# Performance work log

Hardware: AMD Instinct MI355X
Metric: run time of the kernel (lower is better)

Reference implementation:

```python
import jax, jax.numpy as jnp
import numpy as np

B, S, D = 4, 2048, 1024  # batch, seq_len, d_model == d_internal


def setup_inputs() -> dict:
    key = jax.random.key(0)
    ks = jax.random.split(key, 7)
    s = 1.0 / np.sqrt(D)  # scale weights so softmax / relu stay in a sane range
    return {
        "input_vecs": jax.random.normal(ks[0], (B, S, D), jnp.float32),
        "Wq": jax.random.normal(ks[1], (D, D), jnp.float32) * s,
        "Wk": jax.random.normal(ks[2], (D, D), jnp.float32) * s,
        "Wv": jax.random.normal(ks[3], (D, D), jnp.float32) * s,
        "W1": jax.random.normal(ks[4], (D, D), jnp.float32) * s,  # linear1: d_internal -> d_model
        "b1": jnp.zeros((D,), jnp.float32),
        "W2": jax.random.normal(ks[5], (D, D), jnp.float32) * s,  # linear2: d_model -> d_internal
        "b2": jnp.zeros((D,), jnp.float32),
    }


def reference(input_vecs, Wq, Wk, Wv, W1, b1, W2, b2):
    d_internal = Wq.shape[1]
    # single-head self-attention: Q,K,V = X @ Wq/Wk/Wv
    q = jnp.einsum("bsd,de->bse", input_vecs, Wq)
    k = jnp.einsum("bsd,de->bse", input_vecs, Wk)
    v = jnp.einsum("bsd,de->bse", input_vecs, Wv)
    scores = jnp.einsum("bqe,bke->bqk", q, k) / jnp.sqrt(jnp.asarray(d_internal, q.dtype))
    attn = jax.nn.softmax(scores, axis=-1)               # [B, S, S]
    attn_out = jnp.einsum("bqk,bke->bqe", attn, v)       # [B, S, D]
    h = attn_out + input_vecs                            # residual 1
    h = jax.nn.relu(h @ W1 + b1)                         # linear1 + relu
    out = h @ W2 + b2 + input_vecs                       # linear2 + residual 2
    return out, attn
```

## Files before the change

kernel.cpp:

```cpp
#include <hip/hip_runtime.h>
#include <hip/hip_bf16.h>

typedef unsigned short u16;
typedef unsigned int   u32;
typedef u16   u16x8 __attribute__((ext_vector_type(8)));
typedef u16   u16x4 __attribute__((ext_vector_type(4)));
typedef __bf16 bf16x8 __attribute__((ext_vector_type(8)));
typedef float f32x4 __attribute__((ext_vector_type(4)));

__device__ __forceinline__ u16 f2bf(float f) {
    u32 u = __float_as_uint(f);
    u = u + 0x7FFFu + ((u >> 16) & 1u);
    return (u16)(u >> 16);
}
__device__ __forceinline__ float bf2f(u16 b) {
    return __uint_as_float((u32)b << 16);
}

__device__ __forceinline__ void gload16(const u16* g, u16* l) {
    __builtin_amdgcn_global_load_lds(
        (const __attribute__((address_space(1))) void*)g,
        (__attribute__((address_space(3))) void*)l,
        16, 0, 0);
}

#define WAITV(N) asm volatile("s_waitcnt vmcnt(" #N ")" ::: "memory")
#define SCHEDB() __builtin_amdgcn_sched_barrier(0)
#define BAR()    __builtin_amdgcn_s_barrier()

__global__ __launch_bounds__(256) void cvt_x(const float* __restrict__ X,
                                             u16* __restrict__ Xb) {
    const long i = (long)(blockIdx.x * 256 + threadIdx.x) * 8;
    float4 a = *(const float4*)(X + i);
    float4 b = *(const float4*)(X + i + 4);
    u16x8 r;
    r[0] = f2bf(a.x); r[1] = f2bf(a.y); r[2] = f2bf(a.z); r[3] = f2bf(a.w);
    r[4] = f2bf(b.x); r[5] = f2bf(b.y); r[6] = f2bf(b.z); r[7] = f2bf(b.w);
    *(u16x8*)(Xb + i) = r;
}

__global__ __launch_bounds__(256) void cvt_wT(const float* __restrict__ w0,
                                              const float* __restrict__ w1,
                                              const float* __restrict__ w2,
                                              const float* __restrict__ w3,
                                              const float* __restrict__ w4,
                                              u16* __restrict__ wt) {
    const float* srcs[5] = {w0, w1, w2, w3, w4};
    const float* W = srcs[blockIdx.z];
    u16* WT = wt + (long)blockIdx.z * 1048576;
    __shared__ float t[32][33];
    const int tx = threadIdx.x, ty = threadIdx.y;
    const int n0 = blockIdx.x * 32, k0 = blockIdx.y * 32;
    #pragma unroll
    for (int r = 0; r < 4; ++r)
        t[ty + 8 * r][tx] = W[(long)(k0 + ty + 8 * r) * 1024 + n0 + tx];
    __syncthreads();
    #pragma unroll
    for (int r = 0; r < 4; ++r)
        WT[(long)(n0 + ty + 8 * r) * 1024 + k0 + tx] = f2bf(t[tx][ty + 8 * r]);
}

enum { EPI_QKV = 0, EPI_ADDX_BF16 = 3,
       EPI_BIAS_RELU_BF16 = 4, EPI_BIAS_ADDX_F32 = 5 };

#define BM3 256
#define BN3 128
#define BK3 32
#define S3_A (BM3 * BK3)
#define S3_B (BN3 * BK3)
#define S3SZ (S3_A + S3_B)

__global__ __launch_bounds__(512, 2)
void gemm_bt32(const u16* __restrict__ A, const u16* __restrict__ Bt,
               void* __restrict__ Cout, void* __restrict__ CoutK,
               void* __restrict__ CoutV,
               const int M, const int N, const int K,
               const long sA, const long sB,
               const float scale) {
    const int GX = gridDim.x, GY = gridDim.y;
    const int p  = blockIdx.x + GX * (blockIdx.y + GY * blockIdx.z);
    const int slab = (p & 7) + 8 * (p / (8 * GY));
    const int vy   = (p >> 3) % GY;
    const int vx   = slab % GX;
    const int bz   = slab / GX;

    const u16* Ab = A + (long)bz * sA;
    const u16* Bb = Bt + (long)bz * sB;

    const int tid  = threadIdx.x;
    const int lane = tid & 63;
    const int w    = tid >> 6;
    const int wrg  = (w >> 1) * 64;
    const int wcg  = (w & 1) * 64;
    const int m0   = vx * BM3;
    const int n0   = vy * BN3;

    __shared__ __align__(16) u16 LDS[3 * S3SZ];

    f32x4 acc[4][4] = {};

    const long Kl = K;
    const int schunk = ((lane & 3) ^ ((lane >> 3) & 3)) * 8;
    const u16* Ag = Ab + (long)(m0 + w * 32 + (lane >> 2)) * Kl + schunk;
    const u16* Bg = Bb + (long)(n0 + w * 16 + (lane >> 2)) * Kl + schunk;

    const int rbase = lane & 15;
    const int koff  = ((lane >> 4) ^ ((rbase >> 1) & 3)) * 8;

    const int dAoff = (w * 32) * BK3;
    const int dBoff = S3_A + (w * 16) * BK3;

    #define LDA3(mi) (*(const bf16x8*)(Asl + (wrg + (mi) * 16 + rbase) * BK3 + koff))
    #define LDB3(ni) (*(const bf16x8*)(Bsl + (wcg + (ni) * 16 + rbase) * BK3 + koff))
    #define STAGE3(KT, SLOT) do {                                  \
        u16* a_ = &LDS[(SLOT) * S3SZ + dAoff];                     \
        u16* b_ = &LDS[(SLOT) * S3SZ + dBoff];                     \
        gload16(Ag + (KT), a_);                                    \
        gload16(Ag + (KT) + 16 * Kl, a_ + 16 * BK3);               \
        gload16(Bg + (KT), b_);                                    \
    } while (0)

    const int nt = K / BK3;
    STAGE3(0, 0);
    STAGE3(BK3, 1);
    WAITV(3);
    BAR();

    int s = 0;
    for (int t = 0; t < nt; ++t) {
        const u16* Asl = &LDS[s * S3SZ];
        const u16* Bsl = &LDS[s * S3SZ + S3_A];
        const int s2 = (s + 2 >= 3) ? s - 1 : s + 2;
        const bool st = (t + 2 < nt);

        if (st) STAGE3((long)(t + 2) * BK3, s2);

        bf16x8 af[4], bf[4];
        #pragma unroll
        for (int mi = 0; mi < 4; ++mi) af[mi] = LDA3(mi);
        #pragma unroll
        for (int ni = 0; ni < 4; ++ni) bf[ni] = LDB3(ni);
        #pragma unroll
        for (int mi = 0; mi < 4; ++mi)
            #pragma unroll
            for (int ni = 0; ni < 4; ++ni)
                acc[mi][ni] = __builtin_amdgcn_mfma_f32_16x16x32_bf16(
                    af[mi], bf[ni], acc[mi][ni], 0, 0, 0);

        SCHEDB();
        if (st) { WAITV(3); } else { WAITV(0); }
        BAR();
        SCHEDB();
        s = (s == 2) ? 0 : s + 1;
    }
    #undef LDA3
    #undef LDB3
    #undef STAGE3

    const int colb = wcg + (lane & 15);
    const int rq   = (lane >> 4) * 4;
    #pragma unroll
    for (int mi = 0; mi < 4; ++mi) {
        #pragma unroll
        for (int ni = 0; ni < 4; ++ni) {
            f32x4 v = acc[mi][ni];
            const int gr0 = m0 + wrg + mi * 16 + rq;
            const int gc  = n0 + colb + ni * 16;
            if (bz == 2) {
                u16x4 p2;
                p2[0] = f2bf(v[0]); p2[1] = f2bf(v[1]);
                p2[2] = f2bf(v[2]); p2[3] = f2bf(v[3]);
                u16* C = (u16*)CoutV;
                const long off = ((long)(gr0 >> 11)) * 2097152 +
                                 (long)gc * 2048 + (gr0 & 2047);
                *(u16x4*)(C + off) = p2;
            } else {
                u16* C = (u16*)(bz == 0 ? Cout : CoutK);
                #pragma unroll
                for (int j = 0; j < 4; ++j)
                    C[(long)(gr0 + j) * N + gc] = f2bf(v[j]);
            }
        }
    }
}

#define GBM 256
#define GBN 256
#define GBK 64
#define GSLOT_A (GBM * GBK)
#define GSLOTSZ (2 * GSLOT_A)

__global__ __launch_bounds__(512, 1)
void gemm_big(const u16* __restrict__ A, const u16* __restrict__ Bt,
              u16* __restrict__ SbLo, u16* __restrict__ SbHi,
              const int N, const int K,
              const long sA, const long sB,
              const float scale) {
    const int GX = gridDim.x, GY = gridDim.y;
    const int p  = blockIdx.x + GX * (blockIdx.y + GY * blockIdx.z);
    const int slab = (p & 7) + 8 * (p / (8 * GY));
    const int vy   = (p >> 3) % GY;
    const int vx   = slab % GX;
    const int bz   = slab / GX;

    const u16* Ab = A + (long)bz * sA;
    const u16* Bb = Bt + (long)bz * sB;

    const int tid  = threadIdx.x;
    const int lane = tid & 63;
    const int w    = tid >> 6;
    const int wrg  = (w >> 2) * 128;
    const int wcg  = (w & 3) * 64;
    const int m0   = vx * GBM;
    const int n0   = vy * GBN;

    __shared__ __align__(16) u16 LDS[2 * GSLOTSZ];

    f32x4 acc[8][4] = {};

    const long Kl = K;
    const int schunk = ((lane & 7) ^ (lane >> 3)) * 8;
    const u16* Ag = Ab + (long)(m0 + w * 32 + (lane >> 3)) * Kl + schunk;
    const u16* Bg = Bb + (long)(n0 + w * 32 + (lane >> 3)) * Kl + schunk;

    const int rbase = lane & 15;
    const int rx    = rbase & 7;
    const int q4    = lane >> 4;

    const int dAoff = (w * 32) * GBK;
    const int dBoff = GSLOT_A + (w * 32) * GBK;

    #define GLDA(mi, ks) (*(const bf16x8*)(Asl + (wrg + (mi) * 16 + rbase) * GBK \
                          + ((((ks) * 4 + q4) ^ rx)) * 8))
    #define GLDB(ni, ks) (*(const bf16x8*)(Bsl + (wcg + (ni) * 16 + rbase) * GBK \
                          + ((((ks) * 4 + q4) ^ rx)) * 8))
    #define GSTAGE_A(KT, D) do {                       \
        gload16(Ag + (KT), (D));                       \
        gload16(Ag + (KT) + 8 * Kl,  (D) + 512);       \
        gload16(Ag + (KT) + 16 * Kl, (D) + 1024);      \
        gload16(Ag + (KT) + 24 * Kl, (D) + 1536);      \
    } while (0)
    #define GSTAGE_B(KT, D) do {                       \
        gload16(Bg + (KT), (D));                       \
        gload16(Bg + (KT) + 8 * Kl,  (D) + 512);       \
        gload16(Bg + (KT) + 16 * Kl, (D) + 1024);      \
        gload16(Bg + (KT) + 24 * Kl, (D) + 1536);      \
    } while (0)

    const int nt = K / GBK;
    GSTAGE_A(0, &LDS[0] + dAoff);
    GSTAGE_B(0, &LDS[0] + dBoff);
    WAITV(0);
    BAR();

    for (int t = 0; t < nt; ++t) {
        const int s = t & 1;
        const u16* Asl = &LDS[s * GSLOTSZ];
        const u16* Bsl = &LDS[s * GSLOTSZ] + GSLOT_A;
        u16* dnx = &LDS[(s ^ 1) * GSLOTSZ];
        const bool st = (t + 1 < nt);
        const long kt1 = (long)(t + 1) * GBK;

        if (st) {
            GSTAGE_A(kt1, dnx + dAoff);
            GSTAGE_B(kt1, dnx + dBoff);
        }

        bf16x8 bf[4][2];
        #pragma unroll
        for (int ni = 0; ni < 4; ++ni) {
            bf[ni][0] = GLDB(ni, 0);
            bf[ni][1] = GLDB(ni, 1);
        }
        bf16x8 a0 = GLDA(0, 0), a1 = GLDA(0, 1);
        #pragma unroll
        for (int mi = 0; mi < 8; ++mi) {
            bf16x8 c0 = a0, c1 = a1;
            if (mi < 7) { a0 = GLDA(mi + 1, 0); a1 = GLDA(mi + 1, 1); }
            #pragma unroll
            for (int ni = 0; ni < 4; ++ni) {
                acc[mi][ni] = __builtin_amdgcn_mfma_f32_16x16x32_bf16(
                    c0, bf[ni][0], acc[mi][ni], 0, 0, 0);
                acc[mi][ni] = __builtin_amdgcn_mfma_f32_16x16x32_bf16(
                    c1, bf[ni][1], acc[mi][ni], 0, 0, 0);
            }
        }

        SCHEDB();
        WAITV(0);
        BAR();
        SCHEDB();
    }
    #undef GLDA
    #undef GLDB
    #undef GSTAGE_A
    #undef GSTAGE_B

    u16* Sb = (bz < 2 ? SbLo : SbHi) + (long)(bz & 1) * 4194304;
    const int colb = wcg + (lane & 15);
    const int rq   = (lane >> 4) * 4;
    #pragma unroll
    for (int mi = 0; mi < 8; ++mi) {
        #pragma unroll
        for (int ni = 0; ni < 4; ++ni) {
            f32x4 v = acc[mi][ni];
            const int gr0 = m0 + wrg + mi * 16 + rq;
            const int gc  = n0 + colb + ni * 16;
            #pragma unroll
            for (int j = 0; j < 4; ++j)
                Sb[(long)(gr0 + j) * N + gc] = f2bf(v[j] * scale);
        }
    }
}

#define BML 256
#define BNL 128
#define BKW 64
#define LSLOT_A (BML * BKW)
#define LSLOT_B (BNL * BKW)
#define LSLOTSZ (LSLOT_A + LSLOT_B)

template <int EPI>
__global__ __launch_bounds__(512, 1)
void gemm_bt(const u16* __restrict__ A, const u16* __restrict__ Bt,
             void* __restrict__ Cout,
             const float* __restrict__ bias, const float* __restrict__ Xres,
             const int M, const int N, const int K,
             const long sA, const long sB, const long sC, const long sX,
             const float scale) {
    const int GX = gridDim.x, GY = gridDim.y;
    const int p  = blockIdx.x + GX * (blockIdx.y + GY * blockIdx.z);
    const int slab = (p & 7) + 8 * (p / (8 * GY));
    const int vy   = (p >> 3) % GY;
    const int vx   = slab % GX;
    const int bz   = slab / GX;

    const u16* Ab = A + (long)bz * sA;
    const u16* Bb = Bt + (long)bz * sB;
    const float* Xr = Xres ? Xres + (long)bz * sX : nullptr;

    const int tid  = threadIdx.x;
    const int lane = tid & 63;
    const int w    = tid >> 6;
    const int wrg  = (w >> 1) * 64;
    const int wcg  = (w & 1) * 64;
    const int m0   = vx * BML;
    const int n0   = vy * BNL;

    __shared__ __align__(16) u16 LDS[3 * LSLOTSZ];

    f32x4 acc[4][4] = {};

    const long Kl = K;
    const int schunk = ((lane & 7) ^ (lane >> 3)) * 8;
    const u16* Ag = Ab + (long)(m0 + w * 32 + (lane >> 3)) * Kl + schunk;
    const u16* Bg = Bb + (long)(n0 + w * 16 + (lane >> 3)) * Kl + schunk;

    const int rbase = lane & 15;
    const int rx    = rbase & 7;
    const int q4    = lane >> 4;

    const int dAoff = (w * 32) * BKW;
    const int dBoff = LSLOT_A + (w * 16) * BKW;

    #define LDAL(mi, ks) (*(const bf16x8*)(Asl + (wrg + (mi) * 16 + rbase) * BKW \
                         + ((((ks) * 4 + q4) ^ rx)) * 8))
    #define LDBL(ni, ks) (*(const bf16x8*)(Bsl + (wcg + (ni) * 16 + rbase) * BKW \
                         + ((((ks) * 4 + q4) ^ rx)) * 8))

    const int nt = K / BKW;
    {
        u16* d0 = &LDS[0];
        gload16(Ag, d0 + dAoff);
        gload16(Ag + 8 * Kl,  d0 + dAoff + 512);
        gload16(Ag + 16 * Kl, d0 + dAoff + 1024);
        gload16(Ag + 24 * Kl, d0 + dAoff + 1536);
        gload16(Bg, d0 + dBoff);
        gload16(Bg + 8 * Kl,  d0 + dBoff + 512);
        u16* d1 = &LDS[LSLOTSZ];
        gload16(Ag + BKW, d1 + dAoff);
        gload16(Ag + BKW + 8 * Kl,  d1 + dAoff + 512);
        gload16(Ag + BKW + 16 * Kl, d1 + dAoff + 1024);
        gload16(Ag + BKW + 24 * Kl, d1 + dAoff + 1536);
        gload16(Bg + BKW, d1 + dBoff);
        gload16(Bg + BKW + 8 * Kl,  d1 + dBoff + 512);
    }
    WAITV(6);
    BAR();

    int s = 0;
    for (int t = 0; t < nt; ++t) {
        const u16* Asl = &LDS[s * LSLOTSZ];
        const u16* Bsl = &LDS[s * LSLOTSZ + LSLOT_A];
        const int s2 = (s + 2 >= 3) ? s - 1 : s + 2;
        u16* dA = &LDS[s2 * LSLOTSZ] + dAoff;
        u16* dB = &LDS[s2 * LSLOTSZ] + dBoff;
        const bool st = (t + 2 < nt);
        const long kt2 = (long)(t + 2) * BKW;

        if (st) {
            gload16(Ag + kt2, dA);
            gload16(Ag + kt2 + 8 * Kl,  dA + 512);
            gload16(Ag + kt2 + 16 * Kl, dA + 1024);
            gload16(Ag + kt2 + 24 * Kl, dA + 1536);
            gload16(Bg + kt2, dB);
            gload16(Bg + kt2 + 8 * Kl,  dB + 512);
        }

        bf16x8 af[4][2], bf[4][2];
        #pragma unroll
        for (int mi = 0; mi < 4; ++mi) {
            af[mi][0] = LDAL(mi, 0);
            af[mi][1] = LDAL(mi, 1);
        }
        #pragma unroll
        for (int ni = 0; ni < 4; ++ni) {
            bf[ni][0] = LDBL(ni, 0);
            bf[ni][1] = LDBL(ni, 1);
        }
        #pragma unroll
        for (int ks = 0; ks < 2; ++ks)
            #pragma unroll
            for (int mi = 0; mi < 4; ++mi)
                #pragma unroll
                for (int ni = 0; ni < 4; ++ni)
                    acc[mi][ni] = __builtin_amdgcn_mfma_f32_16x16x32_bf16(
                        af[mi][ks], bf[ni][ks], acc[mi][ni], 0, 0, 0);

        SCHEDB();
        if (st) { WAITV(6); } else { WAITV(0); }
        BAR();
        SCHEDB();
        s = (s == 2) ? 0 : s + 1;
    }
    #undef LDAL
    #undef LDBL

    const int colb = wcg + (lane & 15);
    const int rq   = (lane >> 4) * 4;
    #pragma unroll
    for (int mi = 0; mi < 4; ++mi) {
        #pragma unroll
        for (int ni = 0; ni < 4; ++ni) {
            f32x4 v = acc[mi][ni];
            const int gr0 = m0 + wrg + mi * 16 + rq;
            const int gc  = n0 + colb + ni * 16;
            #pragma unroll
            for (int j = 0; j < 4; ++j) {
                const long idx = (long)(gr0 + j) * N + gc;
                float val = v[j];
                if constexpr (EPI == EPI_ADDX_BF16) {
                    val += Xr[idx];
                    ((u16*)Cout + (long)bz * sC)[idx] = f2bf(val);
                } else if constexpr (EPI == EPI_BIAS_RELU_BF16) {
                    val = fmaxf(val + bias[gc], 0.0f);
                    ((u16*)Cout + (long)bz * sC)[idx] = f2bf(val);
                } else if constexpr (EPI == EPI_BIAS_ADDX_F32) {
                    ((float*)Cout + (long)bz * sC)[idx] =
                        val + bias[gc] + Xr[idx];
                }
            }
        }
    }
}

__global__ __launch_bounds__(256)
void softmax_rows(const u16* __restrict__ SbLo, const u16* __restrict__ SbHi,
                  float* __restrict__ attn, u16* __restrict__ P) {
    const int row  = blockIdx.x;
    const u16* srow = (row < 4096 ? SbLo + (long)row * 2048
                                  : SbHi + (long)(row - 4096) * 2048);
    const int tid  = threadIdx.x;
    const int lane = tid & 63;
    const int w    = tid >> 6;

    u16x8 raw = *(const u16x8*)(srow + tid * 8);
    float v[8];
    #pragma unroll
    for (int i = 0; i < 8; ++i) v[i] = bf2f(raw[i]);

    float m = fmaxf(fmaxf(fmaxf(v[0], v[1]), fmaxf(v[2], v[3])),
                    fmaxf(fmaxf(v[4], v[5]), fmaxf(v[6], v[7])));
    #pragma unroll
    for (int o = 32; o > 0; o >>= 1) m = fmaxf(m, __shfl_xor(m, o));
    __shared__ float redm[4];
    if (lane == 0) redm[w] = m;
    __syncthreads();
    m = fmaxf(fmaxf(redm[0], redm[1]), fmaxf(redm[2], redm[3]));

    float e[8];
    #pragma unroll
    for (int i = 0; i < 8; ++i) e[i] = __expf(v[i] - m);
    float s = ((e[0] + e[1]) + (e[2] + e[3])) + ((e[4] + e[5]) + (e[6] + e[7]));
    #pragma unroll
    for (int o = 32; o > 0; o >>= 1) s += __shfl_xor(s, o);
    __shared__ float reds[4];
    if (lane == 0) reds[w] = s;
    __syncthreads();
    s = (reds[0] + reds[1]) + (reds[2] + reds[3]);
    const float inv = 1.0f / s;

    float4 o0, o1;
    o0.x = e[0] * inv; o0.y = e[1] * inv; o0.z = e[2] * inv; o0.w = e[3] * inv;
    o1.x = e[4] * inv; o1.y = e[5] * inv; o1.z = e[6] * inv; o1.w = e[7] * inv;
    float* ap = attn + (long)row * 2048 + tid * 8;
    *(float4*)(ap)     = o0;
    *(float4*)(ap + 4) = o1;

    u16x8 pb;
    pb[0] = f2bf(o0.x); pb[1] = f2bf(o0.y); pb[2] = f2bf(o0.z); pb[3] = f2bf(o0.w);
    pb[4] = f2bf(o1.x); pb[5] = f2bf(o1.y); pb[6] = f2bf(o1.z); pb[7] = f2bf(o1.w);
    *(u16x8*)(P + (long)row * 2048 + tid * 8) = pb;
}

extern "C" void kernel_launch(void* const* d_in, const int* in_sizes, int n_in,
                              void* d_out, int out_size, void* d_ws, size_t ws_size,
                              hipStream_t stream) {
    const float* X  = (const float*)d_in[0];
    const float* Wq = (const float*)d_in[1];
    const float* Wk = (const float*)d_in[2];
    const float* Wv = (const float*)d_in[3];
    const float* W1 = (const float*)d_in[4];
    const float* b1 = (const float*)d_in[5];
    const float* W2 = (const float*)d_in[6];
    const float* b2 = (const float*)d_in[7];

    float* out  = (float*)d_out;
    float* attn = out + (size_t)8388608;

    char* ws = (char*)d_ws;
    u16* Xb  = (u16*)(ws);
    u16* Qb  = (u16*)(ws + (size_t)16 * 1024 * 1024);
    u16* Kb  = (u16*)(ws + (size_t)32 * 1024 * 1024);
    u16* VT  = (u16*)(ws + (size_t)48 * 1024 * 1024);
    u16* H1b = (u16*)(ws + (size_t)64 * 1024 * 1024);
    u16* WTs = (u16*)(ws + (size_t)80 * 1024 * 1024);
    u16* W1T = WTs + (size_t)3 * 1048576;
    u16* W2T = WTs + (size_t)4 * 1048576;
    u16* SbLo = Xb;
    u16* SbHi = H1b;
    u16* Pb  = Xb;
    u16* Hb  = Kb;

    cvt_x<<<4096, 256, 0, stream>>>(X, Xb);
    cvt_wT<<<dim3(32, 32, 5), dim3(32, 8), 0, stream>>>(Wq, Wk, Wv, W1, W2, WTs);

    gemm_bt32<<<dim3(32, 8, 3), 512, 0, stream>>>(
        Xb, WTs, Qb, Kb, VT, 8192, 1024, 1024, 0, 1048576, 1.0f);

    gemm_big<<<dim3(8, 8, 4), 512, 0, stream>>>(
        Qb, Kb, SbLo, SbHi, 2048, 1024,
        2048L * 1024, 2048L * 1024, 0.03125f);

    softmax_rows<<<8192, 256, 0, stream>>>(SbLo, SbHi, attn, Pb);

    gemm_bt<EPI_ADDX_BF16><<<dim3(8, 8, 4), 512, 0, stream>>>(
        Pb, VT, Hb, nullptr, X, 2048, 1024, 2048,
        2048L * 2048, 1024L * 2048, 2048L * 1024, 2048L * 1024, 1.0f);

    gemm_bt<EPI_BIAS_RELU_BF16><<<dim3(32, 8, 1), 512, 0, stream>>>(
        Hb, W1T, H1b, b1, nullptr, 8192, 1024, 1024, 0, 0, 0, 0, 1.0f);

    gemm_bt<EPI_BIAS_ADDX_F32><<<dim3(32, 8, 1), 512, 0, stream>>>(
        H1b, W2T, out, b2, X, 8192, 1024, 1024, 0, 0, 0, 0, 1.0f);
}
```

Before: 228.6 us.

## Merge conversion kernels, add double-buffered QKV GEMM, reuse 3-stage kernel for scores

Combines the X conversion and the weight-transpose kernels into one launch to cut launch overhead. Adds a new two-stage double-buffered QKV GEMM (gemm_qkv3) that targets six blocks per CU and moves the previous three-stage kernel, now templated, onto the QK^T scores GEMM with 256x128 tiles in place of the 256x256 gemm_big. Smaller score tiles raise block count and occupancy but lower data reuse per block. The new QKV kernel also needs more blocks resident at once to hide its shallower pipeline.

```diff
diff --git a/kernel.cpp b/kernel.cpp
--- a/kernel.cpp
+++ b/kernel.cpp
@@ -28,29 +28,32 @@
 #define SCHEDB() __builtin_amdgcn_sched_barrier(0)
 #define BAR()    __builtin_amdgcn_s_barrier()
 
-__global__ __launch_bounds__(256) void cvt_x(const float* __restrict__ X,
-                                             u16* __restrict__ Xb) {
-    const long i = (long)(blockIdx.x * 256 + threadIdx.x) * 8;
-    float4 a = *(const float4*)(X + i);
-    float4 b = *(const float4*)(X + i + 4);
-    u16x8 r;
-    r[0] = f2bf(a.x); r[1] = f2bf(a.y); r[2] = f2bf(a.z); r[3] = f2bf(a.w);
-    r[4] = f2bf(b.x); r[5] = f2bf(b.y); r[6] = f2bf(b.z); r[7] = f2bf(b.w);
-    *(u16x8*)(Xb + i) = r;
-}
-
-__global__ __launch_bounds__(256) void cvt_wT(const float* __restrict__ w0,
-                                              const float* __restrict__ w1,
-                                              const float* __restrict__ w2,
-                                              const float* __restrict__ w3,
-                                              const float* __restrict__ w4,
-                                              u16* __restrict__ wt) {
+__global__ __launch_bounds__(256)
+void cvt_all(const float* __restrict__ X, u16* __restrict__ Xb,
+             const float* __restrict__ w0, const float* __restrict__ w1,
+             const float* __restrict__ w2, const float* __restrict__ w3,
+             const float* __restrict__ w4, u16* __restrict__ wt) {
+    const int bx  = blockIdx.x;
+    const int tid = threadIdx.x;
+    if (bx < 4096) {
+        const long i = (long)(bx * 256 + tid) * 8;
+        float4 a = *(const float4*)(X + i);
+        float4 b = *(const float4*)(X + i + 4);
+        u16x8 r;
+        r[0] = f2bf(a.x); r[1] = f2bf(a.y); r[2] = f2bf(a.z); r[3] = f2bf(a.w);
+        r[4] = f2bf(b.x); r[5] = f2bf(b.y); r[6] = f2bf(b.z); r[7] = f2bf(b.w);
+        *(u16x8*)(Xb + i) = r;
+        return;
+    }
+    const int wb  = bx - 4096;
+    const int wz  = wb >> 10;
+    const int rem = wb & 1023;
     const float* srcs[5] = {w0, w1, w2, w3, w4};
-    const float* W = srcs[blockIdx.z];
-    u16* WT = wt + (long)blockIdx.z * 1048576;
+    const float* W = srcs[wz];
+    u16* WT = wt + (long)wz * 1048576;
     __shared__ float t[32][33];
-    const int tx = threadIdx.x, ty = threadIdx.y;
-    const int n0 = blockIdx.x * 32, k0 = blockIdx.y * 32;
+    const int tx = tid & 31, ty = tid >> 5;
+    const int n0 = (rem & 31) * 32, k0 = (rem >> 5) * 32;
     #pragma unroll
     for (int r = 0; r < 4; ++r)
         t[ty + 8 * r][tx] = W[(long)(k0 + ty + 8 * r) * 1024 + n0 + tx];
@@ -60,7 +63,7 @@
         WT[(long)(n0 + ty + 8 * r) * 1024 + k0 + tx] = f2bf(t[tx][ty + 8 * r]);
 }
 
-enum { EPI_QKV = 0, EPI_ADDX_BF16 = 3,
+enum { EPI_QKV = 0, EPI_SCORES = 1, EPI_ADDX_BF16 = 3,
        EPI_BIAS_RELU_BF16 = 4, EPI_BIAS_ADDX_F32 = 5 };
 
 #define BM3 256
@@ -70,6 +73,7 @@
 #define S3_B (BN3 * BK3)
 #define S3SZ (S3_A + S3_B)
 
+template <int EPI>
 __global__ __launch_bounds__(512, 2)
 void gemm_bt32(const u16* __restrict__ A, const u16* __restrict__ Bt,
                void* __restrict__ Cout, void* __restrict__ CoutK,
@@ -152,6 +156,124 @@
         BAR();
         SCHEDB();
         s = (s == 2) ? 0 : s + 1;
+    }
+    #undef LDA3
+    #undef LDB3
+    #undef STAGE3
+
+    const int colb = wcg + (lane & 15);
+    const int rq   = (lane >> 4) * 4;
+    #pragma unroll
+    for (int mi = 0; mi < 4; ++mi) {
+        #pragma unroll
+        for (int ni = 0; ni < 4; ++ni) {
+            f32x4 v = acc[mi][ni];
+            const int gr0 = m0 + wrg + mi * 16 + rq;
+            const int gc  = n0 + colb + ni * 16;
+            if constexpr (EPI == EPI_QKV) {
+                if (bz == 2) {
+                    u16x4 p2;
+                    p2[0] = f2bf(v[0]); p2[1] = f2bf(v[1]);
+                    p2[2] = f2bf(v[2]); p2[3] = f2bf(v[3]);
+                    u16* C = (u16*)CoutV;
+                    const long off = ((long)(gr0 >> 11)) * 2097152 +
+                                     (long)gc * 2048 + (gr0 & 2047);
+                    *(u16x4*)(C + off) = p2;
+                } else {
+                    u16* C = (u16*)(bz == 0 ? Cout : CoutK);
+                    #pragma unroll
+                    for (int j = 0; j < 4; ++j)
+                        C[(long)(gr0 + j) * N + gc] = f2bf(v[j]);
+                }
+            } else if constexpr (EPI == EPI_SCORES) {
+                u16* Sb = (u16*)(bz < 2 ? Cout : CoutK) + (long)(bz & 1) * 4194304;
+                #pragma unroll
+                for (int j = 0; j < 4; ++j)
+                    Sb[(long)(gr0 + j) * N + gc] = f2bf(v[j] * scale);
+            }
+        }
+    }
+}
+
+__global__ __launch_bounds__(512, 6)
+void gemm_qkv3(const u16* __restrict__ A, const u16* __restrict__ Bt,
+               void* __restrict__ Cout, void* __restrict__ CoutK,
+               void* __restrict__ CoutV,
+               const int M, const int N, const int K,
+               const long sA, const long sB,
+               const float scale) {
+    const int GX = gridDim.x, GY = gridDim.y;
+    const int p  = blockIdx.x + GX * (blockIdx.y + GY * blockIdx.z);
+    const int slab = (p & 7) + 8 * (p / (8 * GY));
+    const int vy   = (p >> 3) % GY;
+    const int vx   = slab % GX;
+    const int bz   = slab / GX;
+
+    const u16* Ab = A + (long)bz * sA;
+    const u16* Bb = Bt + (long)bz * sB;
+
+    const int tid  = threadIdx.x;
+    const int lane = tid & 63;
+    const int w    = tid >> 6;
+    const int wrg  = (w >> 1) * 64;
+    const int wcg  = (w & 1) * 64;
+    const int m0   = vx * BM3;
+    const int n0   = vy * BN3;
+
+    __shared__ __align__(16) u16 LDS[2 * S3SZ];
+
+    f32x4 acc[4][4] = {};
+
+    const long Kl = K;
+    const int schunk = ((lane & 3) ^ ((lane >> 3) & 3)) * 8;
+    const u16* Ag = Ab + (long)(m0 + w * 32 + (lane >> 2)) * Kl + schunk;
+    const u16* Bg = Bb + (long)(n0 + w * 16 + (lane >> 2)) * Kl + schunk;
+
+    const int rbase = lane & 15;
+    const int koff  = ((lane >> 4) ^ ((rbase >> 1) & 3)) * 8;
+
+    const int dAoff = (w * 32) * BK3;
+    const int dBoff = S3_A + (w * 16) * BK3;
+
+    #define LDA3(mi) (*(const bf16x8*)(Asl + (wrg + (mi) * 16 + rbase) * BK3 + koff))
+    #define LDB3(ni) (*(const bf16x8*)(Bsl + (wcg + (ni) * 16 + rbase) * BK3 + koff))
+    #define STAGE3(KT, SLOT) do {                                  \
+        u16* a_ = &LDS[(SLOT) * S3SZ + dAoff];                     \
+        u16* b_ = &LDS[(SLOT) * S3SZ + dBoff];                     \
+        gload16(Ag + (KT), a_);                                    \
+        gload16(Ag + (KT) + 16 * Kl, a_ + 16 * BK3);               \
+        gload16(Bg + (KT), b_);                                    \
+    } while (0)
+
+    const int nt = K / BK3;
+    STAGE3(0, 0);
+    WAITV(0);
+    BAR();
+
+    for (int t = 0; t < nt; ++t) {
+        const int s = t & 1;
+        const u16* Asl = &LDS[s * S3SZ];
+        const u16* Bsl = &LDS[s * S3SZ + S3_A];
+        const bool st = (t + 1 < nt);
+
+        if (st) STAGE3((long)(t + 1) * BK3, s ^ 1);
+
+        bf16x8 af[4], bf[4];
+        #pragma unroll
+        for (int mi = 0; mi < 4; ++mi) af[mi] = LDA3(mi);
+        #pragma unroll
+        for (int ni = 0; ni < 4; ++ni) bf[ni] = LDB3(ni);
+        #pragma unroll
+        for (int mi = 0; mi < 4; ++mi)
+            #pragma unroll
+            for (int ni = 0; ni < 4; ++ni)
+                acc[mi][ni] = __builtin_amdgcn_mfma_f32_16x16x32_bf16(
+                    af[mi], bf[ni], acc[mi][ni], 0, 0, 0);
+
+        SCHEDB();
+        WAITV(0);
+        BAR();
+        SCHEDB();
     }
     #undef LDA3
     #undef LDB3
@@ -180,135 +302,6 @@
                 for (int j = 0; j < 4; ++j)
                     C[(long)(gr0 + j) * N + gc] = f2bf(v[j]);
             }
-        }
-    }
-}
-
-#define GBM 256
-#define GBN 256
-#define GBK 64
-#define GSLOT_A (GBM * GBK)
-#define GSLOTSZ (2 * GSLOT_A)
-
-__global__ __launch_bounds__(512, 1)
-void gemm_big(const u16* __restrict__ A, const u16* __restrict__ Bt,
-              u16* __restrict__ SbLo, u16* __restrict__ SbHi,
-              const int N, const int K,
-              const long sA, const long sB,
-              const float scale) {
-    const int GX = gridDim.x, GY = gridDim.y;
-    const int p  = blockIdx.x + GX * (blockIdx.y + GY * blockIdx.z);
-    const int slab = (p & 7) + 8 * (p / (8 * GY));
-    const int vy   = (p >> 3) % GY;
-    const int vx   = slab % GX;
-    const int bz   = slab / GX;
-
-    const u16* Ab = A + (long)bz * sA;
-    const u16* Bb = Bt + (long)bz * sB;
-
-    const int tid  = threadIdx.x;
-    const int lane = tid & 63;
-    const int w    = tid >> 6;
-    const int wrg  = (w >> 2) * 128;
-    const int wcg  = (w & 3) * 64;
-    const int m0   = vx * GBM;
-    const int n0   = vy * GBN;
-
-    __shared__ __align__(16) u16 LDS[2 * GSLOTSZ];
-
-    f32x4 acc[8][4] = {};
-
-    const long Kl = K;
-    const int schunk = ((lane & 7) ^ (lane >> 3)) * 8;
-    const u16* Ag = Ab + (long)(m0 + w * 32 + (lane >> 3)) * Kl + schunk;
-    const u16* Bg = Bb + (long)(n0 + w * 32 + (lane >> 3)) * Kl + schunk;
-
-    const int rbase = lane & 15;
-    const int rx    = rbase & 7;
-    const int q4    = lane >> 4;
-
-    const int dAoff = (w * 32) * GBK;
-    const int dBoff = GSLOT_A + (w * 32) * GBK;
-
-    #define GLDA(mi, ks) (*(const bf16x8*)(Asl + (wrg + (mi) * 16 + rbase) * GBK \
-                          + ((((ks) * 4 + q4) ^ rx)) * 8))
-    #define GLDB(ni, ks) (*(const bf16x8*)(Bsl + (wcg + (ni) * 16 + rbase) * GBK \
-                          + ((((ks) * 4 + q4) ^ rx)) * 8))
-    #define GSTAGE_A(KT, D) do {                       \
-        gload16(Ag + (KT), (D));                       \
-        gload16(Ag + (KT) + 8 * Kl,  (D) + 512);       \
-        gload16(Ag + (KT) + 16 * Kl, (D) + 1024);      \
-        gload16(Ag + (KT) + 24 * Kl, (D) + 1536);      \
-    } while (0)
-    #define GSTAGE_B(KT, D) do {                       \
-        gload16(Bg + (KT), (D));                       \
-        gload16(Bg + (KT) + 8 * Kl,  (D) + 512);       \
-        gload16(Bg + (KT) + 16 * Kl, (D) + 1024);      \
-        gload16(Bg + (KT) + 24 * Kl, (D) + 1536);      \
-    } while (0)
-
-    const int nt = K / GBK;
-    GSTAGE_A(0, &LDS[0] + dAoff);
-    GSTAGE_B(0, &LDS[0] + dBoff);
-    WAITV(0);
-    BAR();
-
-    for (int t = 0; t < nt; ++t) {
-        const int s = t & 1;
-        const u16* Asl = &LDS[s * GSLOTSZ];
-        const u16* Bsl = &LDS[s * GSLOTSZ] + GSLOT_A;
-        u16* dnx = &LDS[(s ^ 1) * GSLOTSZ];
-        const bool st = (t + 1 < nt);
-        const long kt1 = (long)(t + 1) * GBK;
-
-        if (st) {
-            GSTAGE_A(kt1, dnx + dAoff);
-            GSTAGE_B(kt1, dnx + dBoff);
-        }
-
-        bf16x8 bf[4][2];
-        #pragma unroll
-        for (int ni = 0; ni < 4; ++ni) {
-            bf[ni][0] = GLDB(ni, 0);
-            bf[ni][1] = GLDB(ni, 1);
-        }
-        bf16x8 a0 = GLDA(0, 0), a1 = GLDA(0, 1);
-        #pragma unroll
-        for (int mi = 0; mi < 8; ++mi) {
-            bf16x8 c0 = a0, c1 = a1;
-            if (mi < 7) { a0 = GLDA(mi + 1, 0); a1 = GLDA(mi + 1, 1); }
-            #pragma unroll
-            for (int ni = 0; ni < 4; ++ni) {
-                acc[mi][ni] = __builtin_amdgcn_mfma_f32_16x16x32_bf16(
-                    c0, bf[ni][0], acc[mi][ni], 0, 0, 0);
-                acc[mi][ni] = __builtin_amdgcn_mfma_f32_16x16x32_bf16(
-                    c1, bf[ni][1], acc[mi][ni], 0, 0, 0);
-            }
-        }
-
-        SCHEDB();
-        WAITV(0);
-        BAR();
-        SCHEDB();
-    }
-    #undef GLDA
-    #undef GLDB
-    #undef GSTAGE_A
-    #undef GSTAGE_B
-
-    u16* Sb = (bz < 2 ? SbLo : SbHi) + (long)(bz & 1) * 4194304;
-    const int colb = wcg + (lane & 15);
-    const int rq   = (lane >> 4) * 4;
-    #pragma unroll
-    for (int mi = 0; mi < 8; ++mi) {
-        #pragma unroll
-        for (int ni = 0; ni < 4; ++ni) {
-            f32x4 v = acc[mi][ni];
-            const int gr0 = m0 + wrg + mi * 16 + rq;
-            const int gc  = n0 + colb + ni * 16;
-            #pragma unroll
-            for (int j = 0; j < 4; ++j)
-                Sb[(long)(gr0 + j) * N + gc] = f2bf(v[j] * scale);
         }
     }
 }
@@ -542,14 +535,13 @@
     u16* Pb  = Xb;
     u16* Hb  = Kb;
 
-    cvt_x<<<4096, 256, 0, stream>>>(X, Xb);
-    cvt_wT<<<dim3(32, 32, 5), dim3(32, 8), 0, stream>>>(Wq, Wk, Wv, W1, W2, WTs);
-
-    gemm_bt32<<<dim3(32, 8, 3), 512, 0, stream>>>(
+    cvt_all<<<9216, 256, 0, stream>>>(X, Xb, Wq, Wk, Wv, W1, W2, WTs);
+
+    gemm_qkv3<<<dim3(32, 8, 3), 512, 0, stream>>>(
         Xb, WTs, Qb, Kb, VT, 8192, 1024, 1024, 0, 1048576, 1.0f);
 
-    gemm_big<<<dim3(8, 8, 4), 512, 0, stream>>>(
-        Qb, Kb, SbLo, SbHi, 2048, 1024,
+    gemm_bt32<EPI_SCORES><<<dim3(8, 16, 4), 512, 0, stream>>>(
+        Qb, Kb, SbLo, SbHi, nullptr, 2048, 2048, 1024,
         2048L * 1024, 2048L * 1024, 0.03125f);
 
     softmax_rows<<<8192, 256, 0, stream>>>(SbLo, SbHi, attn, Pb);
```

Measured after the change: 430.0 us. 88.1% more time.
